# Optimization experiments

Measured on AMD Instinct MI355X. Metric: run time of the kernel, lower is better.

Reference implementation:

```python
import jax, jax.numpy as jnp
import numpy as np

K = 40        # nearest neighbors
BN_EPS = 1e-5  # nn.BatchNorm1d default eps


def _bn(x, g, b):
    # training-mode BatchNorm1d: batch mean, biased variance
    mu = x.mean(0)
    var = x.var(0)
    return g * (x - mu) / jnp.sqrt(var + BN_EPS) + b


def setup_inputs() -> dict:
    key = jax.random.key(0)
    ks = jax.random.split(key, 16)
    N, Cin, D, S, P = 8192, 16, 32, 3, 32

    def w(k, i, o):
        return jax.random.normal(k, (i, o), jnp.float32) * (1.0 / np.sqrt(i))

    return {
        "x": jax.random.normal(ks[0], (N, Cin), jnp.float32),
        "original_coords": jax.random.normal(ks[1], (N, 3), jnp.float32),
        "batch": jnp.zeros((N,), jnp.int32),
        "step_count": 0,
        "num_layer": 1,
        # pre_gravnet MLP
        "pre_w1": w(ks[2], Cin, D), "pre_b1": jnp.zeros((D,), jnp.float32),
        "pre_w2": w(ks[3], D, D), "pre_b2": jnp.zeros((D,), jnp.float32),
        "bn1_g": jnp.ones((D,), jnp.float32), "bn1_b": jnp.zeros((D,), jnp.float32),
        # GravNetConv projections
        "lin_s_w": w(ks[4], D, S),
        "lin_h_w": w(ks[5], D, P), "lin_h_b": jnp.zeros((P,), jnp.float32),
        "lin_w": w(ks[6], D + 2 * P, D), "lin_b": jnp.zeros((D,), jnp.float32),
        # post_gravnet MLP (in = out_channels + space_dims + d_shape = 32+3+32)
        "post_w1": w(ks[7], D + S + D, D), "post_b1": jnp.zeros((D,), jnp.float32),
        "post_w2": w(ks[8], D, D), "post_b2": jnp.zeros((D,), jnp.float32),
        "bn2_g": jnp.ones((D,), jnp.float32), "bn2_b": jnp.zeros((D,), jnp.float32),
    }


def reference(x, original_coords, batch, step_count, num_layer,
              pre_w1, pre_b1, pre_w2, pre_b2, bn1_g, bn1_b,
              lin_s_w, lin_h_w, lin_h_b, lin_w, lin_b,
              post_w1, post_b1, post_w2, post_b2, bn2_g, bn2_b):
    N = x.shape[0]

    # pre_gravnet MLP + batchnorm
    h = jax.nn.elu(x @ pre_w1 + pre_b1)
    h = jax.nn.elu(h @ pre_w2 + pre_b2)
    x_in = _bn(h, bn1_g, bn1_b)

    # GravNetConv projections
    h_l = x_in @ lin_h_w + lin_h_b          # [N, P] propagated features
    s_l = x_in @ lin_s_w                    # [N, S] learned coordinate space

    # kNN graph in s-space (self loops excluded)
    sq = jnp.sum(s_l * s_l, axis=1)
    d2 = sq[:, None] + sq[None, :] - 2.0 * (s_l @ s_l.T)   # [N, N]
    d2 = jnp.maximum(d2, 0.0)
    d2 = jnp.where(jnp.eye(N, dtype=bool), jnp.inf, d2)
    _, idx = jax.lax.top_k(-d2, K)           # [N, K] neighbor indices

    # per-edge squared distance (NOTE: propagate uses the SQUARED distance,
    # faithful to the source where edge_weight is never re-bound to sqrt)
    edge_sq = jnp.take_along_axis(d2, idx, axis=1)    # [N, K]
    dist = jnp.sqrt(edge_sq + 1e-6)                   # [N, K]

    # DGL-side reductions at dst = edge_index[1] = neighbor index
    dst = idx.reshape(-1)
    distf = dist.reshape(-1)
    indeg = jax.ops.segment_sum(jnp.ones_like(distf), dst, num_segments=N)
    sum_d = jax.ops.segment_sum(distf, dst, num_segments=N)
    avdist = jnp.where(indeg > 0, sum_d / jnp.maximum(indeg, 1.0), 0.0)
    loss_regularizing_neig = 0.01 * jnp.mean(jnp.square(avdist - 0.5))

    norm_d = distf / (sum_d + 1e-4)[dst]              # EdgeWeightNorm('right')
    # faithful to source bug: '_edge_w_gndist' is set to the NORMALIZED dist,
    # and apply_edges multiplies by the RAW '_edge_w'
    degs2 = jax.ops.segment_sum(norm_d, dst, num_segments=N) + 1e-4
    gn_final = distf / degs2[dst]
    loss_llregulariser = 0.1 * jnp.mean(jnp.square(norm_d - gn_final))

    # message passing: msg = h_l[neighbor] * squared_dist, mean+max over the
    # K neighbors of each source node (regular fan-in -> dense reduce)
    msgs = h_l[idx] * edge_sq[..., None]              # [N, K, P]
    agg = jnp.concatenate([msgs.mean(1), msgs.max(1)], axis=-1)  # [N, 2P]
    xgn = jnp.concatenate([agg, x_in], axis=-1) @ lin_w + lin_b   # [N, 32]

    # post_gravnet MLP + batchnorm
    cat = jnp.concatenate([xgn, s_l, x_in], axis=1)   # [N, 67]
    o = jax.nn.elu(cat @ post_w1 + post_b1)
    o = jax.nn.elu(o @ post_w2 + post_b2)
    out = _bn(o, bn2_g, bn2_b)
    return (out, loss_regularizing_neig, loss_llregulariser)
```

## Files before the change

### kernel.cpp

```cpp
#include <hip/hip_runtime.h>
#include <math.h>

#define NPTS 8192
#define KNN 40
#define DD 32
#define CIN 16
#define RPB 8
#define CAP 96

#define OFF_H      0u
#define OFF_XIN    262144u
#define OFF_HL     524288u
#define OFF_SL     786432u
#define OFF_ESQ    819200u
#define OFF_O      1146880u
#define OFF_IDX    1409024u
#define OFF_SUMD   1736704u
#define OFF_INDEG  1744896u
#define OFF_STATS  1753088u
#define ZERO_FLOATS (8192u + 8192u + 130u * 32u)

#define ST(i) stats[(i) * 32]

__device__ __forceinline__ float elu_f(float x) { return x > 0.f ? x : (expf(x) - 1.f); }

__device__ __forceinline__ float grp_sum32(float v) {
#pragma unroll
    for (int m = 1; m < 32; m <<= 1) v += __shfl_xor(v, m);
    return v;
}

__device__ __forceinline__ unsigned fkey(float x) {
    unsigned b = __float_as_uint(x);
    return b ^ ((unsigned)((int)b >> 31) | 0x80000000u);
}
__device__ __forceinline__ float kinv(unsigned k) {
    unsigned b = (k & 0x80000000u) ? (k ^ 0x80000000u) : ~k;
    return __uint_as_float(b);
}

__device__ __forceinline__ unsigned bisect_kth(unsigned u0, unsigned u1, int kth) {
    unsigned lo = 0u, hi = 0xFFFFFFFFu;
    while (lo < hi) {
        unsigned mid = lo + ((hi - lo) >> 1);
        int cnt = __popcll(__ballot(u0 <= mid)) + __popcll(__ballot(u1 <= mid));
        if (cnt >= kth) hi = mid; else lo = mid + 1;
    }
    return hi;
}

__global__ __launch_bounds__(256) void k_pre(const float* __restrict__ x,
    const float* __restrict__ w1, const float* __restrict__ b1,
    const float* __restrict__ w2, const float* __restrict__ b2,
    float* __restrict__ h, float* __restrict__ stats)
{
    __shared__ float sw1[CIN * DD], sw2[DD * DD], sb1[DD], sb2[DD];
    __shared__ float bufx[RPB][20], buft[RPB][36];
    __shared__ float sstat[2 * DD];
    int tid = threadIdx.x;
    for (int t = tid; t < CIN * DD; t += 256) sw1[t] = w1[t];
    for (int t = tid; t < DD * DD; t += 256) sw2[t] = w2[t];
    if (tid < DD) { sb1[tid] = b1[tid]; sb2[tid] = b2[tid]; }
    if (tid < 2 * DD) sstat[tid] = 0.f;

    int r = tid >> 5, ch = tid & 31;
    int g = blockIdx.x * RPB + r;
    if (ch < CIN) bufx[r][ch] = x[(size_t)g * CIN + ch];
    __syncthreads();

    float acc = sb1[ch];
#pragma unroll
    for (int k4 = 0; k4 < CIN; k4 += 4) {
        float4 v = *(const float4*)&bufx[r][k4];
        acc = fmaf(v.x, sw1[(k4 + 0) * DD + ch], acc);
        acc = fmaf(v.y, sw1[(k4 + 1) * DD + ch], acc);
        acc = fmaf(v.z, sw1[(k4 + 2) * DD + ch], acc);
        acc = fmaf(v.w, sw1[(k4 + 3) * DD + ch], acc);
    }
    acc = elu_f(acc);
    buft[r][ch] = acc;
    __syncthreads();

    float o = sb2[ch];
#pragma unroll
    for (int k4 = 0; k4 < DD; k4 += 4) {
        float4 v = *(const float4*)&buft[r][k4];
        o = fmaf(v.x, sw2[(k4 + 0) * DD + ch], o);
        o = fmaf(v.y, sw2[(k4 + 1) * DD + ch], o);
        o = fmaf(v.z, sw2[(k4 + 2) * DD + ch], o);
        o = fmaf(v.w, sw2[(k4 + 3) * DD + ch], o);
    }
    o = elu_f(o);
    h[(size_t)g * DD + ch] = o;

    float s = o + __shfl_xor(o, 32);
    float q = o * o;
    q += __shfl_xor(q, 32);
    if ((tid & 32) == 0) { atomicAdd(&sstat[ch], s); atomicAdd(&sstat[DD + ch], q); }
    __syncthreads();
    if (tid < 2 * DD) atomicAdd(&ST(tid), sstat[tid]);
}

__global__ __launch_bounds__(256) void k_proj(const float* __restrict__ h,
    const float* __restrict__ stats,
    const float* __restrict__ g1, const float* __restrict__ b1g,
    const float* __restrict__ hw, const float* __restrict__ hb,
    const float* __restrict__ sw,
    float* __restrict__ xin, float* __restrict__ hl, float4* __restrict__ sl4)
{
    __shared__ float shw[DD * DD], ssw[DD * 3], sa[DD], sbp[DD], shb[DD];
    __shared__ float rrow[RPB][36];
    int tid = threadIdx.x;
    for (int t = tid; t < DD * DD; t += 256) shw[t] = hw[t];
    if (tid < DD * 3) ssw[tid] = sw[tid];
    if (tid < DD) {
        float mean = ST(tid) * (1.f / NPTS);
        float var = ST(32 + tid) * (1.f / NPTS) - mean * mean;
        float a = g1[tid] * rsqrtf(var + 1e-5f);
        sa[tid] = a;
        sbp[tid] = b1g[tid] - a * mean;
        shb[tid] = hb[tid];
    }
    __syncthreads();

    int r = tid >> 5, ch = tid & 31;
    int g = blockIdx.x * RPB + r;

    float v = fmaf(sa[ch], h[(size_t)g * DD + ch], sbp[ch]);
    xin[(size_t)g * DD + ch] = v;
    rrow[r][ch] = v;

    float p0 = v * ssw[ch * 3 + 0];
    float p1 = v * ssw[ch * 3 + 1];
    float p2 = v * ssw[ch * 3 + 2];
    p0 = grp_sum32(p0); p1 = grp_sum32(p1); p2 = grp_sum32(p2);
    if (ch == 0) sl4[g] = make_float4(p0, p1, p2, 0.5f * (p0 * p0 + p1 * p1 + p2 * p2));
    __syncthreads();

    float o = shb[ch];
#pragma unroll
    for (int k4 = 0; k4 < DD; k4 += 4) {
        float4 vv = *(const float4*)&rrow[r][k4];
        o = fmaf(vv.x, shw[(k4 + 0) * DD + ch], o);
        o = fmaf(vv.y, shw[(k4 + 1) * DD + ch], o);
        o = fmaf(vv.z, shw[(k4 + 2) * DD + ch], o);
        o = fmaf(vv.w, shw[(k4 + 3) * DD + ch], o);
    }
    hl[(size_t)g * DD + ch] = o;
}

__device__ __forceinline__ void select_emit(const float2* bufq, int C, int qidx,
    float qw, int lane, int* __restrict__ idxo, float* __restrict__ esq,
    float* __restrict__ sumd, float* __restrict__ indeg)
{
    float e0 = INFINITY, e1 = INFINITY;
    int j0 = -1, j1 = -1;
    if (lane < C) { float2 t = bufq[lane]; e0 = t.x; j0 = __float_as_int(t.y); }
    if (lane + 64 < C) { float2 t = bufq[lane + 64]; e1 = t.x; j1 = __float_as_int(t.y); }
    if (j0 == qidx) e0 = INFINITY;
    if (j1 == qidx) e1 = INFINITY;
    unsigned u0 = fkey(e0), u1 = fkey(e1);
    unsigned thr = bisect_kth(u0, u1, KNN);
    unsigned long long ltm = (1ull << lane) - 1;
    unsigned long long mlt0 = __ballot(u0 < thr), mlt1 = __ballot(u1 < thr);
    unsigned long long meq0 = __ballot(u0 == thr), meq1 = __ballot(u1 == thr);
    int nlt = __popcll(mlt0) + __popcll(mlt1);
    int need = KNN - nlt;
    int rb = qidx * KNN;

    int pos = -1;
    if (u0 < thr) pos = __popcll(mlt0 & ltm);
    else if (u0 == thr) { int rk = __popcll(meq0 & ltm); if (rk < need) pos = nlt + rk; }
    if (pos >= 0) {
        float d2 = fmaxf(2.f * (e0 + qw), 0.f);
        idxo[rb + pos] = j0; esq[rb + pos] = d2;
        float dist = sqrtf(d2 + 1e-6f);
        atomicAdd(&sumd[j0], dist); atomicAdd(&indeg[j0], 1.f);
    }
    pos = -1;
    if (u1 < thr) pos = __popcll(mlt0) + __popcll(mlt1 & ltm);
    else if (u1 == thr) {
        int rk = __popcll(meq0) + __popcll(meq1 & ltm);
        if (rk < need) pos = nlt + rk;
    }
    if (pos >= 0) {
        float d2 = fmaxf(2.f * (e1 + qw), 0.f);
        idxo[rb + pos] = j1; esq[rb + pos] = d2;
        float dist = sqrtf(d2 + 1e-6f);
        atomicAdd(&sumd[j1], dist); atomicAdd(&indeg[j1], 1.f);
    }
}

__global__ __launch_bounds__(256) void k_knn(const float4* __restrict__ sl4,
    int* __restrict__ idxo, float* __restrict__ esq,
    float* __restrict__ sumd, float* __restrict__ indeg)
{
    __shared__ float2 buf[8][CAP];
    int tid = threadIdx.x, lane = tid & 63, wid = tid >> 6;
    int qai = blockIdx.x * 8 + wid * 2;
    int qbi = qai + 1;
    float4 qa = sl4[qai], qb = sl4[qbi];

    float m0a = INFINITY, m1a = INFINITY, m0b = INFINITY, m1b = INFINITY;
    for (int base = 0; base < NPTS; base += 64) {
        float4 p = sl4[base + lane];
        float ea = fmaf(-qa.x, p.x, fmaf(-qa.y, p.y, fmaf(-qa.z, p.z, p.w)));
        float eb = fmaf(-qb.x, p.x, fmaf(-qb.y, p.y, fmaf(-qb.z, p.z, p.w)));
        float lo = fminf(ea, m0a), hi = fmaxf(ea, m0a);
        m0a = lo; m1a = fminf(m1a, hi);
        lo = fminf(eb, m0b); hi = fmaxf(eb, m0b);
        m0b = lo; m1b = fminf(m1b, hi);
    }
    float thrfa = kinv(bisect_kth(fkey(m0a), fkey(m1a), KNN + 1));
    float thrfb = kinv(bisect_kth(fkey(m0b), fkey(m1b), KNN + 1));

    unsigned long long ltm = (1ull << lane) - 1;
    int ca = 0, cbn = 0;
    float2* bufa = buf[wid * 2];
    float2* bufb = buf[wid * 2 + 1];
    for (int base = 0; base < NPTS; base += 64) {
        float4 p = sl4[base + lane];
        int jj = base + lane;
        float ea = fmaf(-qa.x, p.x, fmaf(-qa.y, p.y, fmaf(-qa.z, p.z, p.w)));
        float eb = fmaf(-qb.x, p.x, fmaf(-qb.y, p.y, fmaf(-qb.z, p.z, p.w)));
        unsigned long long ma = __ballot(ea <= thrfa);
        unsigned long long mb = __ballot(eb <= thrfb);
        if (ma) {
            if (ea <= thrfa) {
                int pos = ca + __popcll(ma & ltm);
                if (pos < CAP) bufa[pos] = make_float2(ea, __int_as_float(jj));
            }
            ca += __popcll(ma);
        }
        if (mb) {
            if (eb <= thrfb) {
                int pos = cbn + __popcll(mb & ltm);
                if (pos < CAP) bufb[pos] = make_float2(eb, __int_as_float(jj));
            }
            cbn += __popcll(mb);
        }
    }
    __syncthreads();

    select_emit(bufa, ca < CAP ? ca : CAP, qai, qa.w, lane, idxo, esq, sumd, indeg);
    select_emit(bufb, cbn < CAP ? cbn : CAP, qbi, qb.w, lane, idxo, esq, sumd, indeg);
}

__global__ __launch_bounds__(256) void k_agg(
    const int* __restrict__ idx, const float* __restrict__ esq,
    const float* __restrict__ hl, const float* __restrict__ xin,
    const float4* __restrict__ sl4,
    const float* __restrict__ sumd, const float* __restrict__ indeg,
    const float* __restrict__ lw, const float* __restrict__ lb,
    const float* __restrict__ pw1, const float* __restrict__ pb1,
    const float* __restrict__ pw2, const float* __restrict__ pb2,
    float* __restrict__ o, float* __restrict__ stats)
{
    __shared__ float slw[96 * DD], spw1[67 * DD], spw2[DD * DD];
    __shared__ float slb[DD], spb1[DD], spb2[DD];
    __shared__ float rbuf[RPB][100];
    __shared__ float rb2[RPB][68];
    __shared__ float sstat[2 * DD];
    __shared__ float sl1, sl2;
    int tid = threadIdx.x;
    for (int t = tid; t < 96 * DD; t += 256) slw[t] = lw[t];
    for (int t = tid; t < 67 * DD; t += 256) spw1[t] = pw1[t];
    for (int t = tid; t < DD * DD; t += 256) spw2[t] = pw2[t];
    if (tid < DD) { slb[tid] = lb[tid]; spb1[tid] = pb1[tid]; spb2[tid] = pb2[tid]; }
    if (tid < 2 * DD) sstat[tid] = 0.f;
    if (tid == 254) sl1 = 0.f;
    if (tid == 255) sl2 = 0.f;

    int r = tid >> 5, ch = tid & 31;
    int g = blockIdx.x * RPB + r;
    int rb = g * KNN;

    float sv = 0.f, mv = -INFINITY;
#pragma unroll 8
    for (int k = 0; k < KNN; ++k) {
        int j = idx[rb + k];
        float w = esq[rb + k];
        float m = hl[(size_t)j * DD + ch] * w;
        sv += m;
        mv = fmaxf(mv, m);
    }
    rbuf[r][ch] = sv * (1.f / KNN);
    rbuf[r][32 + ch] = mv;
    rbuf[r][64 + ch] = xin[(size_t)g * DD + ch];
    if (ch == 0) { float4 s = sl4[g]; rbuf[r][96] = s.x; rbuf[r][97] = s.y; rbuf[r][98] = s.z; }
    __syncthreads();

    float l2 = 0.f;
    {
        int j = idx[rb + ch];
        float w = esq[rb + ch];
        float dist = sqrtf(w + 1e-6f);
        float sd = sumd[j];
        float r1 = 1.f / (sd + 1e-4f);
        float dg = sd * r1 + 1e-4f;
        float df = dist * r1 - dist / dg;
        l2 = df * df;
        if (ch < KNN - 32) {
            j = idx[rb + 32 + ch];
            w = esq[rb + 32 + ch];
            dist = sqrtf(w + 1e-6f);
            sd = sumd[j];
            r1 = 1.f / (sd + 1e-4f);
            dg = sd * r1 + 1e-4f;
            df = dist * r1 - dist / dg;
            l2 += df * df;
        }
    }
    l2 = grp_sum32(l2);
    if (ch == 0) {
        float id = indeg[g], sdg = sumd[g];
        float av = id > 0.f ? sdg / fmaxf(id, 1.f) : 0.f;
        float dd = av - 0.5f;
        atomicAdd(&sl2, l2);
        atomicAdd(&sl1, dd * dd);
    }

    float acc = slb[ch];
#pragma unroll
    for (int k4 = 0; k4 < 96; k4 += 4) {
        float4 v = *(const float4*)&rbuf[r][k4];
        acc = fmaf(v.x, slw[(k4 + 0) * DD + ch], acc);
        acc = fmaf(v.y, slw[(k4 + 1) * DD + ch], acc);
        acc = fmaf(v.z, slw[(k4 + 2) * DD + ch], acc);
        acc = fmaf(v.w, slw[(k4 + 3) * DD + ch], acc);
    }
    rb2[r][ch] = acc;
    __syncthreads();

    acc = spb1[ch];
#pragma unroll
    for (int k4 = 0; k4 < DD; k4 += 4) {
        float4 v = *(const float4*)&rb2[r][k4];
        acc = fmaf(v.x, spw1[(k4 + 0) * DD + ch], acc);
        acc = fmaf(v.y, spw1[(k4 + 1) * DD + ch], acc);
        acc = fmaf(v.z, spw1[(k4 + 2) * DD + ch], acc);
        acc = fmaf(v.w, spw1[(k4 + 3) * DD + ch], acc);
    }
#pragma unroll
    for (int s2 = 0; s2 < 3; ++s2)
        acc = fmaf(rbuf[r][96 + s2], spw1[(32 + s2) * DD + ch], acc);
#pragma unroll
    for (int k4 = 0; k4 < DD; k4 += 4) {
        float4 v = *(const float4*)&rbuf[r][64 + k4];
        acc = fmaf(v.x, spw1[(35 + k4 + 0) * DD + ch], acc);
        acc = fmaf(v.y, spw1[(35 + k4 + 1) * DD + ch], acc);
        acc = fmaf(v.z, spw1[(35 + k4 + 2) * DD + ch], acc);
        acc = fmaf(v.w, spw1[(35 + k4 + 3) * DD + ch], acc);
    }
    acc = elu_f(acc);
    rb2[r][32 + ch] = acc;
    __syncthreads();

    acc = spb2[ch];
#pragma unroll
    for (int k4 = 0; k4 < DD; k4 += 4) {
        float4 v = *(const float4*)&rb2[r][32 + k4];
        acc = fmaf(v.x, spw2[(k4 + 0) * DD + ch], acc);
        acc = fmaf(v.y, spw2[(k4 + 1) * DD + ch], acc);
        acc = fmaf(v.z, spw2[(k4 + 2) * DD + ch], acc);
        acc = fmaf(v.w, spw2[(k4 + 3) * DD + ch], acc);
    }
    acc = elu_f(acc);
    o[(size_t)g * DD + ch] = acc;

    float s = acc + __shfl_xor(acc, 32);
    float q = acc * acc;
    q += __shfl_xor(q, 32);
    if ((tid & 32) == 0) { atomicAdd(&sstat[ch], s); atomicAdd(&sstat[DD + ch], q); }
    __syncthreads();
    if (tid < 2 * DD) atomicAdd(&ST(64 + tid), sstat[tid]);
    if (tid == 0) { atomicAdd(&ST(128), sl1); atomicAdd(&ST(129), sl2); }
}

__global__ __launch_bounds__(256) void k_out(const float* __restrict__ o,
    const float* __restrict__ stats, const float* __restrict__ g,
    const float* __restrict__ b, float* __restrict__ dout)
{
    __shared__ float sa[DD], sb[DD];
    int tid = threadIdx.x;
    if (tid < DD) {
        float mean = ST(64 + tid) * (1.f / NPTS);
        float var = ST(96 + tid) * (1.f / NPTS) - mean * mean;
        float a = g[tid] * rsqrtf(var + 1e-5f);
        sa[tid] = a;
        sb[tid] = b[tid] - a * mean;
    }
    __syncthreads();

    int t = blockIdx.x * 256 + tid;
    float4 v = ((const float4*)o)[t];
    int cbase = (t * 4) & (DD - 1);
    float4 rr;
    rr.x = fmaf(sa[cbase + 0], v.x, sb[cbase + 0]);
    rr.y = fmaf(sa[cbase + 1], v.y, sb[cbase + 1]);
    rr.z = fmaf(sa[cbase + 2], v.z, sb[cbase + 2]);
    rr.w = fmaf(sa[cbase + 3], v.w, sb[cbase + 3]);
    ((float4*)dout)[t] = rr;

    if (blockIdx.x == 0) {
        if (tid == DD)     dout[NPTS * DD]     = 0.01f * ST(128) * (1.f / NPTS);
        if (tid == DD + 1) dout[NPTS * DD + 1] = 0.1f  * ST(129) * (1.f / ((float)NPTS * KNN));
    }
}

extern "C" void kernel_launch(void* const* d_in, const int* in_sizes, int n_in,
                              void* d_out, int out_size, void* d_ws, size_t ws_size,
                              hipStream_t stream)
{
    (void)in_sizes; (void)n_in; (void)out_size; (void)ws_size;
    const float* x      = (const float*)d_in[0];
    const float* pre_w1 = (const float*)d_in[5];
    const float* pre_b1 = (const float*)d_in[6];
    const float* pre_w2 = (const float*)d_in[7];
    const float* pre_b2 = (const float*)d_in[8];
    const float* bn1_g  = (const float*)d_in[9];
    const float* bn1_b  = (const float*)d_in[10];
    const float* lin_s_w = (const float*)d_in[11];
    const float* lin_h_w = (const float*)d_in[12];
    const float* lin_h_b = (const float*)d_in[13];
    const float* lin_w   = (const float*)d_in[14];
    const float* lin_b   = (const float*)d_in[15];
    const float* post_w1 = (const float*)d_in[16];
    const float* post_b1 = (const float*)d_in[17];
    const float* post_w2 = (const float*)d_in[18];
    const float* post_b2 = (const float*)d_in[19];
    const float* bn2_g   = (const float*)d_in[20];
    const float* bn2_b   = (const float*)d_in[21];

    float* W = (float*)d_ws;
    float* h     = W + OFF_H;
    float* xin   = W + OFF_XIN;
    float* hl    = W + OFF_HL;
    float4* sl4  = (float4*)(W + OFF_SL);
    float* esq   = W + OFF_ESQ;
    float* o     = W + OFF_O;
    int*   idx   = (int*)(W + OFF_IDX);
    float* sumd  = W + OFF_SUMD;
    float* indeg = W + OFF_INDEG;
    float* stats = W + OFF_STATS;
    float* dout  = (float*)d_out;

    hipMemsetAsync(W + OFF_SUMD, 0, ZERO_FLOATS * sizeof(float), stream);

    k_pre<<<NPTS / RPB, 256, 0, stream>>>(x, pre_w1, pre_b1, pre_w2, pre_b2, h, stats);
    k_proj<<<NPTS / RPB, 256, 0, stream>>>(h, stats, bn1_g, bn1_b,
                                           lin_h_w, lin_h_b, lin_s_w, xin, hl, sl4);
    k_knn<<<NPTS / 8, 256, 0, stream>>>(sl4, idx, esq, sumd, indeg);
    k_agg<<<NPTS / RPB, 256, 0, stream>>>(idx, esq, hl, xin, sl4, sumd, indeg,
                                          lin_w, lin_b, post_w1, post_b1, post_w2, post_b2,
                                          o, stats);
    k_out<<<NPTS * DD / 1024, 256, 0, stream>>>(o, stats, bn2_g, bn2_b, dout);
}
```

Baseline: 131.9 us.

## Stage kNN candidate points in double-buffered LDS tiles, four queries per wave

The kNN kernel now loads the point coordinates into a double-buffered shared-memory tile, with register prefetch of the next tile. Each wave processes four queries instead of two, and the block count is halved. The goal is to cut repeated global/L1 loads of the point array and share each load across more queries. In exchange it uses about 76KB of LDS per block and adds block-wide barriers per tile, which may limit occupancy.

```diff
diff --git a/kernel.cpp b/kernel.cpp
--- a/kernel.cpp
+++ b/kernel.cpp
@@ -7,6 +7,7 @@
 #define CIN 16
 #define RPB 8
 #define CAP 96
+#define TILE 2048
 
 #define OFF_H      0u
 #define OFF_XIN    262144u
@@ -191,59 +192,112 @@
     }
 }
 
+#define EDIST(p, qq) fmaf(-(qq).x, (p).x, fmaf(-(qq).y, (p).y, fmaf(-(qq).z, (p).z, (p).w)))
+
 __global__ __launch_bounds__(256) void k_knn(const float4* __restrict__ sl4,
     int* __restrict__ idxo, float* __restrict__ esq,
     float* __restrict__ sumd, float* __restrict__ indeg)
 {
-    __shared__ float2 buf[8][CAP];
+    __shared__ float4 tile[2][TILE];
+    __shared__ float2 buf[16][CAP];
     int tid = threadIdx.x, lane = tid & 63, wid = tid >> 6;
-    int qai = blockIdx.x * 8 + wid * 2;
-    int qbi = qai + 1;
-    float4 qa = sl4[qai], qb = sl4[qbi];
+    int q0 = blockIdx.x * 16 + wid * 4;
+    float4 qa = sl4[q0], qb = sl4[q0 + 1], qc = sl4[q0 + 2], qd = sl4[q0 + 3];
+
+    float4 st[8];
+#pragma unroll
+    for (int k = 0; k < 8; ++k) st[k] = sl4[k * 256 + tid];
+#pragma unroll
+    for (int k = 0; k < 8; ++k) tile[0][k * 256 + tid] = st[k];
+    __syncthreads();
 
     float m0a = INFINITY, m1a = INFINITY, m0b = INFINITY, m1b = INFINITY;
-    for (int base = 0; base < NPTS; base += 64) {
-        float4 p = sl4[base + lane];
-        float ea = fmaf(-qa.x, p.x, fmaf(-qa.y, p.y, fmaf(-qa.z, p.z, p.w)));
-        float eb = fmaf(-qb.x, p.x, fmaf(-qb.y, p.y, fmaf(-qb.z, p.z, p.w)));
-        float lo = fminf(ea, m0a), hi = fmaxf(ea, m0a);
-        m0a = lo; m1a = fminf(m1a, hi);
-        lo = fminf(eb, m0b); hi = fmaxf(eb, m0b);
-        m0b = lo; m1b = fminf(m1b, hi);
+    float m0c = INFINITY, m1c = INFINITY, m0d = INFINITY, m1d = INFINITY;
+
+#define TOP2Q(p, qq, m0, m1) { \
+        float e = EDIST(p, qq); \
+        float lo = fminf(e, m0), hi = fmaxf(e, m0); \
+        m0 = lo; m1 = fminf(m1, hi); }
+
+    for (int t = 0; t < NPTS / TILE; ++t) {
+        if (t + 1 < NPTS / TILE) {
+#pragma unroll
+            for (int k = 0; k < 8; ++k) st[k] = sl4[(t + 1) * TILE + k * 256 + tid];
+        }
+        const float4* tp = tile[t & 1];
+#pragma unroll 4
+        for (int g = 0; g < TILE / 64; ++g) {
+            float4 p = tp[g * 64 + lane];
+            TOP2Q(p, qa, m0a, m1a)
+            TOP2Q(p, qb, m0b, m1b)
+            TOP2Q(p, qc, m0c, m1c)
+            TOP2Q(p, qd, m0d, m1d)
+        }
+        __syncthreads();
+        if (t + 1 < NPTS / TILE) {
+#pragma unroll
+            for (int k = 0; k < 8; ++k) tile[(t + 1) & 1][k * 256 + tid] = st[k];
+        }
+        __syncthreads();
     }
     float thrfa = kinv(bisect_kth(fkey(m0a), fkey(m1a), KNN + 1));
     float thrfb = kinv(bisect_kth(fkey(m0b), fkey(m1b), KNN + 1));
+    float thrfc = kinv(bisect_kth(fkey(m0c), fkey(m1c), KNN + 1));
+    float thrfd = kinv(bisect_kth(fkey(m0d), fkey(m1d), KNN + 1));
 
     unsigned long long ltm = (1ull << lane) - 1;
-    int ca = 0, cbn = 0;
-    float2* bufa = buf[wid * 2];
-    float2* bufb = buf[wid * 2 + 1];
-    for (int base = 0; base < NPTS; base += 64) {
-        float4 p = sl4[base + lane];
-        int jj = base + lane;
-        float ea = fmaf(-qa.x, p.x, fmaf(-qa.y, p.y, fmaf(-qa.z, p.z, p.w)));
-        float eb = fmaf(-qb.x, p.x, fmaf(-qb.y, p.y, fmaf(-qb.z, p.z, p.w)));
-        unsigned long long ma = __ballot(ea <= thrfa);
-        unsigned long long mb = __ballot(eb <= thrfb);
-        if (ma) {
-            if (ea <= thrfa) {
-                int pos = ca + __popcll(ma & ltm);
-                if (pos < CAP) bufa[pos] = make_float2(ea, __int_as_float(jj));
-            }
-            ca += __popcll(ma);
-        }
-        if (mb) {
-            if (eb <= thrfb) {
-                int pos = cbn + __popcll(mb & ltm);
-                if (pos < CAP) bufb[pos] = make_float2(eb, __int_as_float(jj));
-            }
-            cbn += __popcll(mb);
-        }
-    }
-    __syncthreads();
-
-    select_emit(bufa, ca < CAP ? ca : CAP, qai, qa.w, lane, idxo, esq, sumd, indeg);
-    select_emit(bufb, cbn < CAP ? cbn : CAP, qbi, qb.w, lane, idxo, esq, sumd, indeg);
+    int ca = 0, cb = 0, cc = 0, cd = 0;
+    float2* bufa = buf[wid * 4 + 0];
+    float2* bufb = buf[wid * 4 + 1];
+    float2* bufc = buf[wid * 4 + 2];
+    float2* bufd = buf[wid * 4 + 3];
+
+#define COLL(e, thrv, cnt, brow, jj) { \
+        unsigned long long mm = __ballot((e) <= (thrv)); \
+        if (mm) { \
+            if ((e) <= (thrv)) { \
+                int pos = cnt + __popcll(mm & ltm); \
+                if (pos < CAP) brow[pos] = make_float2((e), __int_as_float(jj)); \
+            } \
+            cnt += __popcll(mm); \
+        } }
+
+#pragma unroll
+    for (int k = 0; k < 8; ++k) st[k] = sl4[k * 256 + tid];
+#pragma unroll
+    for (int k = 0; k < 8; ++k) tile[0][k * 256 + tid] = st[k];
+    __syncthreads();
+
+    for (int t = 0; t < NPTS / TILE; ++t) {
+        if (t + 1 < NPTS / TILE) {
+#pragma unroll
+            for (int k = 0; k < 8; ++k) st[k] = sl4[(t + 1) * TILE + k * 256 + tid];
+        }
+        const float4* tp = tile[t & 1];
+        int tbase = t * TILE;
+#pragma unroll 4
+        for (int g = 0; g < TILE / 64; ++g) {
+            float4 p = tp[g * 64 + lane];
+            int jj = tbase + g * 64 + lane;
+            float ea = EDIST(p, qa), eb = EDIST(p, qb);
+            float ec = EDIST(p, qc), ed = EDIST(p, qd);
+            COLL(ea, thrfa, ca, bufa, jj)
+            COLL(eb, thrfb, cb, bufb, jj)
+            COLL(ec, thrfc, cc, bufc, jj)
+            COLL(ed, thrfd, cd, bufd, jj)
+        }
+        __syncthreads();
+        if (t + 1 < NPTS / TILE) {
+#pragma unroll
+            for (int k = 0; k < 8; ++k) tile[(t + 1) & 1][k * 256 + tid] = st[k];
+        }
+        __syncthreads();
+    }
+
+    select_emit(bufa, ca < CAP ? ca : CAP, q0 + 0, qa.w, lane, idxo, esq, sumd, indeg);
+    select_emit(bufb, cb < CAP ? cb : CAP, q0 + 1, qb.w, lane, idxo, esq, sumd, indeg);
+    select_emit(bufc, cc < CAP ? cc : CAP, q0 + 2, qc.w, lane, idxo, esq, sumd, indeg);
+    select_emit(bufd, cd < CAP ? cd : CAP, q0 + 3, qd.w, lane, idxo, esq, sumd, indeg);
 }
 
 __global__ __launch_bounds__(256) void k_agg(
@@ -450,7 +504,7 @@
     k_pre<<<NPTS / RPB, 256, 0, stream>>>(x, pre_w1, pre_b1, pre_w2, pre_b2, h, stats);
     k_proj<<<NPTS / RPB, 256, 0, stream>>>(h, stats, bn1_g, bn1_b,
                                            lin_h_w, lin_h_b, lin_s_w, xin, hl, sl4);
-    k_knn<<<NPTS / 8, 256, 0, stream>>>(sl4, idx, esq, sumd, indeg);
+    k_knn<<<NPTS / 16, 256, 0, stream>>>(sl4, idx, esq, sumd, indeg);
     k_agg<<<NPTS / RPB, 256, 0, stream>>>(idx, esq, hl, xin, sl4, sumd, indeg,
                                           lin_w, lin_b, post_w1, post_b1, post_w2, post_b2,
                                           o, stats);
```

Measured after the change: 147.4 us. +11.7%, slower.

## Split kNN candidate scan across two waves per query pair

Applied to the files above, without the earlier changes.

The kNN kernel now assigns each pair of queries to two wavefronts, each scanning half the points, and merges per-lane top-2 minima through shared memory to compute a joint threshold. Each half then collects candidates into a 64-entry buffer, and one wave per query runs the final selection over both halves. This halves the serial scan length per wave and doubles the grid size to expose more parallelism. The cost is an extra block barrier and a per-half candidate cap of 64, which could drop true neighbours if one half holds many ties near the threshold.

```diff
diff --git a/kernel.cpp b/kernel.cpp
--- a/kernel.cpp
+++ b/kernel.cpp
@@ -6,7 +6,8 @@
 #define DD 32
 #define CIN 16
 #define RPB 8
-#define CAP 96
+#define HALF 4096
+#define CAP2 64
 
 #define OFF_H      0u
 #define OFF_XIN    262144u
@@ -44,6 +45,18 @@
     while (lo < hi) {
         unsigned mid = lo + ((hi - lo) >> 1);
         int cnt = __popcll(__ballot(u0 <= mid)) + __popcll(__ballot(u1 <= mid));
+        if (cnt >= kth) hi = mid; else lo = mid + 1;
+    }
+    return hi;
+}
+
+__device__ __forceinline__ unsigned bisect_kth4(unsigned u0, unsigned u1,
+    unsigned u2, unsigned u3, int kth) {
+    unsigned lo = 0u, hi = 0xFFFFFFFFu;
+    while (lo < hi) {
+        unsigned mid = lo + ((hi - lo) >> 1);
+        int cnt = __popcll(__ballot(u0 <= mid)) + __popcll(__ballot(u1 <= mid))
+                + __popcll(__ballot(u2 <= mid)) + __popcll(__ballot(u3 <= mid));
         if (cnt >= kth) hi = mid; else lo = mid + 1;
     }
     return hi;
@@ -149,14 +162,15 @@
     hl[(size_t)g * DD + ch] = o;
 }
 
-__device__ __forceinline__ void select_emit(const float2* bufq, int C, int qidx,
-    float qw, int lane, int* __restrict__ idxo, float* __restrict__ esq,
+__device__ __forceinline__ void select_emit2(const float2* buf0, int c0,
+    const float2* buf1, int c1, int qidx, float qw, int lane,
+    int* __restrict__ idxo, float* __restrict__ esq,
     float* __restrict__ sumd, float* __restrict__ indeg)
 {
     float e0 = INFINITY, e1 = INFINITY;
     int j0 = -1, j1 = -1;
-    if (lane < C) { float2 t = bufq[lane]; e0 = t.x; j0 = __float_as_int(t.y); }
-    if (lane + 64 < C) { float2 t = bufq[lane + 64]; e1 = t.x; j1 = __float_as_int(t.y); }
+    if (lane < c0) { float2 t = buf0[lane]; e0 = t.x; j0 = __float_as_int(t.y); }
+    if (lane < c1) { float2 t = buf1[lane]; e1 = t.x; j1 = __float_as_int(t.y); }
     if (j0 == qidx) e0 = INFINITY;
     if (j1 == qidx) e1 = INFINITY;
     unsigned u0 = fkey(e0), u1 = fkey(e1);
@@ -191,59 +205,75 @@
     }
 }
 
+#define EDIST(p, qq) fmaf(-(qq).x, (p).x, fmaf(-(qq).y, (p).y, fmaf(-(qq).z, (p).z, (p).w)))
+
 __global__ __launch_bounds__(256) void k_knn(const float4* __restrict__ sl4,
     int* __restrict__ idxo, float* __restrict__ esq,
     float* __restrict__ sumd, float* __restrict__ indeg)
 {
-    __shared__ float2 buf[8][CAP];
+    __shared__ float2 pool[4][2][64];
+    __shared__ float2 cand[4][2][CAP2];
+    __shared__ int cnts[4][2];
     int tid = threadIdx.x, lane = tid & 63, wid = tid >> 6;
-    int qai = blockIdx.x * 8 + wid * 2;
-    int qbi = qai + 1;
+    int p = wid >> 1, h = wid & 1;
+    int qbase = blockIdx.x * 4;
+    int qai = qbase + 2 * p, qbi = qai + 1;
     float4 qa = sl4[qai], qb = sl4[qbi];
+    int pbase = h * HALF;
 
     float m0a = INFINITY, m1a = INFINITY, m0b = INFINITY, m1b = INFINITY;
-    for (int base = 0; base < NPTS; base += 64) {
-        float4 p = sl4[base + lane];
-        float ea = fmaf(-qa.x, p.x, fmaf(-qa.y, p.y, fmaf(-qa.z, p.z, p.w)));
-        float eb = fmaf(-qb.x, p.x, fmaf(-qb.y, p.y, fmaf(-qb.z, p.z, p.w)));
-        float lo = fminf(ea, m0a), hi = fmaxf(ea, m0a);
-        m0a = lo; m1a = fminf(m1a, hi);
-        lo = fminf(eb, m0b); hi = fmaxf(eb, m0b);
-        m0b = lo; m1b = fminf(m1b, hi);
-    }
-    float thrfa = kinv(bisect_kth(fkey(m0a), fkey(m1a), KNN + 1));
-    float thrfb = kinv(bisect_kth(fkey(m0b), fkey(m1b), KNN + 1));
+
+#define TOP2Q(pt, qq, m0, m1) { \
+        float e = EDIST(pt, qq); \
+        float lo = fminf(e, m0), hi = fmaxf(e, m0); \
+        m0 = lo; m1 = fminf(m1, hi); }
+
+    for (int i = 0; i < HALF; i += 64) {
+        float4 pt = sl4[pbase + i + lane];
+        TOP2Q(pt, qa, m0a, m1a)
+        TOP2Q(pt, qb, m0b, m1b)
+    }
+    pool[2 * p][h][lane] = make_float2(m0a, m1a);
+    pool[2 * p + 1][h][lane] = make_float2(m0b, m1b);
+    __syncthreads();
+
+    float2 a0 = pool[2 * p][0][lane], a1 = pool[2 * p][1][lane];
+    float2 b0 = pool[2 * p + 1][0][lane], b1 = pool[2 * p + 1][1][lane];
+    float thra = kinv(bisect_kth4(fkey(a0.x), fkey(a0.y), fkey(a1.x), fkey(a1.y), KNN + 1));
+    float thrb = kinv(bisect_kth4(fkey(b0.x), fkey(b0.y), fkey(b1.x), fkey(b1.y), KNN + 1));
 
     unsigned long long ltm = (1ull << lane) - 1;
-    int ca = 0, cbn = 0;
-    float2* bufa = buf[wid * 2];
-    float2* bufb = buf[wid * 2 + 1];
-    for (int base = 0; base < NPTS; base += 64) {
-        float4 p = sl4[base + lane];
-        int jj = base + lane;
-        float ea = fmaf(-qa.x, p.x, fmaf(-qa.y, p.y, fmaf(-qa.z, p.z, p.w)));
-        float eb = fmaf(-qb.x, p.x, fmaf(-qb.y, p.y, fmaf(-qb.z, p.z, p.w)));
-        unsigned long long ma = __ballot(ea <= thrfa);
-        unsigned long long mb = __ballot(eb <= thrfb);
-        if (ma) {
-            if (ea <= thrfa) {
-                int pos = ca + __popcll(ma & ltm);
-                if (pos < CAP) bufa[pos] = make_float2(ea, __int_as_float(jj));
-            }
-            ca += __popcll(ma);
-        }
-        if (mb) {
-            if (eb <= thrfb) {
-                int pos = cbn + __popcll(mb & ltm);
-                if (pos < CAP) bufb[pos] = make_float2(eb, __int_as_float(jj));
-            }
-            cbn += __popcll(mb);
-        }
-    }
-    __syncthreads();
-
-    select_emit(bufa, ca < CAP ? ca : CAP, qai, qa.w, lane, idxo, esq, sumd, indeg);
-    select_emit(bufb, cbn < CAP ? cbn : CAP, qbi, qb.w, lane, idxo, esq, sumd, indeg);
+    int ca = 0, cb = 0;
+    float2* bufa = cand[2 * p][h];
+    float2* bufb = cand[2 * p + 1][h];
+
+#define COLL(e, thrv, cnt, brow, jj) { \
+        unsigned long long mm = __ballot((e) <= (thrv)); \
+        if (mm) { \
+            if ((e) <= (thrv)) { \
+                int pos = cnt + __popcll(mm & ltm); \
+                if (pos < CAP2) brow[pos] = make_float2((e), __int_as_float(jj)); \
+            } \
+            cnt += __popcll(mm); \
+        } }
+
+    for (int i = 0; i < HALF; i += 64) {
+        float4 pt = sl4[pbase + i + lane];
+        int jj = pbase + i + lane;
+        float ea = EDIST(pt, qa), eb = EDIST(pt, qb);
+        COLL(ea, thra, ca, bufa, jj)
+        COLL(eb, thrb, cb, bufb, jj)
+    }
+    if (lane == 0) {
+        cnts[2 * p][h] = ca < CAP2 ? ca : CAP2;
+        cnts[2 * p + 1][h] = cb < CAP2 ? cb : CAP2;
+    }
+    __syncthreads();
+
+    int qi = qbase + wid;
+    float qw = sl4[qi].w;
+    select_emit2(cand[wid][0], cnts[wid][0], cand[wid][1], cnts[wid][1],
+                 qi, qw, lane, idxo, esq, sumd, indeg);
 }
 
 __global__ __launch_bounds__(256) void k_agg(
@@ -450,7 +480,7 @@
     k_pre<<<NPTS / RPB, 256, 0, stream>>>(x, pre_w1, pre_b1, pre_w2, pre_b2, h, stats);
     k_proj<<<NPTS / RPB, 256, 0, stream>>>(h, stats, bn1_g, bn1_b,
                                            lin_h_w, lin_h_b, lin_s_w, xin, hl, sl4);
-    k_knn<<<NPTS / 8, 256, 0, stream>>>(sl4, idx, esq, sumd, indeg);
+    k_knn<<<NPTS / 4, 256, 0, stream>>>(sl4, idx, esq, sumd, indeg);
     k_agg<<<NPTS / RPB, 256, 0, stream>>>(idx, esq, hl, xin, sl4, sumd, indeg,
                                           lin_w, lin_b, post_w1, post_b1, post_w2, post_b2,
                                           o, stats);
```

Result: faster. 122.6 us (-7.1%).

## Split kNN point scan across waves with 8 queries per wave register tile

Applied to the files above, without the earlier changes.

Reorganises the kNN kernel so each wave scans a quarter of the points for all 8 block queries, instead of all points for 2 queries. Per-lane minima from the four waves are pooled in shared memory to compute each query's candidate threshold, and per-quarter candidate lists are merged in a 4-way selection. This amortises point loads over more queries and shortens each wave's serial loop. In exchange it raises register pressure and lowers per-quarter candidate capacity to 64, which could drop neighbours on skewed distributions.

```diff
diff --git a/kernel.cpp b/kernel.cpp
--- a/kernel.cpp
+++ b/kernel.cpp
@@ -6,7 +6,9 @@
 #define DD 32
 #define CIN 16
 #define RPB 8
-#define CAP 96
+#define QPB 8
+#define QTR 2048
+#define CAP3 64
 
 #define OFF_H      0u
 #define OFF_XIN    262144u
@@ -39,11 +41,13 @@
     return __uint_as_float(b);
 }
 
-__device__ __forceinline__ unsigned bisect_kth(unsigned u0, unsigned u1, int kth) {
+__device__ __forceinline__ unsigned bisect_kth4(unsigned u0, unsigned u1,
+    unsigned u2, unsigned u3, int kth) {
     unsigned lo = 0u, hi = 0xFFFFFFFFu;
     while (lo < hi) {
         unsigned mid = lo + ((hi - lo) >> 1);
-        int cnt = __popcll(__ballot(u0 <= mid)) + __popcll(__ballot(u1 <= mid));
+        int cnt = __popcll(__ballot(u0 <= mid)) + __popcll(__ballot(u1 <= mid))
+                + __popcll(__ballot(u2 <= mid)) + __popcll(__ballot(u3 <= mid));
         if (cnt >= kth) hi = mid; else lo = mid + 1;
     }
     return hi;
@@ -149,101 +153,149 @@
     hl[(size_t)g * DD + ch] = o;
 }
 
-__device__ __forceinline__ void select_emit(const float2* bufq, int C, int qidx,
-    float qw, int lane, int* __restrict__ idxo, float* __restrict__ esq,
+__device__ __forceinline__ void emit_one(unsigned u, int j, float qw,
+    unsigned thr, int nlt, int need, int prelt, int preeq,
+    unsigned long long mlt, unsigned long long meq, unsigned long long ltm,
+    int rb, int* __restrict__ idxo, float* __restrict__ esq,
     float* __restrict__ sumd, float* __restrict__ indeg)
 {
-    float e0 = INFINITY, e1 = INFINITY;
-    int j0 = -1, j1 = -1;
-    if (lane < C) { float2 t = bufq[lane]; e0 = t.x; j0 = __float_as_int(t.y); }
-    if (lane + 64 < C) { float2 t = bufq[lane + 64]; e1 = t.x; j1 = __float_as_int(t.y); }
+    int pos = -1;
+    if (u < thr) pos = prelt + __popcll(mlt & ltm);
+    else if (u == thr) {
+        int rk = preeq + __popcll(meq & ltm);
+        if (rk < need) pos = nlt + rk;
+    }
+    if (pos >= 0) {
+        float e = kinv(u);
+        float d2 = fmaxf(2.f * (e + qw), 0.f);
+        idxo[rb + pos] = j; esq[rb + pos] = d2;
+        float dist = sqrtf(d2 + 1e-6f);
+        atomicAdd(&sumd[j], dist); atomicAdd(&indeg[j], 1.f);
+    }
+}
+
+__device__ __forceinline__ void select_emit4(
+    const float2* b0, int c0, const float2* b1, int c1,
+    const float2* b2, int c2, const float2* b3, int c3,
+    int qidx, float qw, int lane,
+    int* __restrict__ idxo, float* __restrict__ esq,
+    float* __restrict__ sumd, float* __restrict__ indeg)
+{
+    float e0 = INFINITY, e1 = INFINITY, e2 = INFINITY, e3 = INFINITY;
+    int j0 = -1, j1 = -1, j2 = -1, j3 = -1;
+    if (lane < c0) { float2 t = b0[lane]; e0 = t.x; j0 = __float_as_int(t.y); }
+    if (lane < c1) { float2 t = b1[lane]; e1 = t.x; j1 = __float_as_int(t.y); }
+    if (lane < c2) { float2 t = b2[lane]; e2 = t.x; j2 = __float_as_int(t.y); }
+    if (lane < c3) { float2 t = b3[lane]; e3 = t.x; j3 = __float_as_int(t.y); }
     if (j0 == qidx) e0 = INFINITY;
     if (j1 == qidx) e1 = INFINITY;
-    unsigned u0 = fkey(e0), u1 = fkey(e1);
-    unsigned thr = bisect_kth(u0, u1, KNN);
+    if (j2 == qidx) e2 = INFINITY;
+    if (j3 == qidx) e3 = INFINITY;
+    unsigned u0 = fkey(e0), u1 = fkey(e1), u2 = fkey(e2), u3 = fkey(e3);
+    unsigned thr = bisect_kth4(u0, u1, u2, u3, KNN);
     unsigned long long ltm = (1ull << lane) - 1;
     unsigned long long mlt0 = __ballot(u0 < thr), mlt1 = __ballot(u1 < thr);
+    unsigned long long mlt2 = __ballot(u2 < thr), mlt3 = __ballot(u3 < thr);
     unsigned long long meq0 = __ballot(u0 == thr), meq1 = __ballot(u1 == thr);
-    int nlt = __popcll(mlt0) + __popcll(mlt1);
+    unsigned long long meq2 = __ballot(u2 == thr), meq3 = __ballot(u3 == thr);
+    int n0 = __popcll(mlt0), n1 = __popcll(mlt1), n2 = __popcll(mlt2), n3 = __popcll(mlt3);
+    int q0 = __popcll(meq0), q1 = __popcll(meq1), q2 = __popcll(meq2);
+    int nlt = n0 + n1 + n2 + n3;
     int need = KNN - nlt;
     int rb = qidx * KNN;
 
-    int pos = -1;
-    if (u0 < thr) pos = __popcll(mlt0 & ltm);
-    else if (u0 == thr) { int rk = __popcll(meq0 & ltm); if (rk < need) pos = nlt + rk; }
-    if (pos >= 0) {
-        float d2 = fmaxf(2.f * (e0 + qw), 0.f);
-        idxo[rb + pos] = j0; esq[rb + pos] = d2;
-        float dist = sqrtf(d2 + 1e-6f);
-        atomicAdd(&sumd[j0], dist); atomicAdd(&indeg[j0], 1.f);
-    }
-    pos = -1;
-    if (u1 < thr) pos = __popcll(mlt0) + __popcll(mlt1 & ltm);
-    else if (u1 == thr) {
-        int rk = __popcll(meq0) + __popcll(meq1 & ltm);
-        if (rk < need) pos = nlt + rk;
-    }
-    if (pos >= 0) {
-        float d2 = fmaxf(2.f * (e1 + qw), 0.f);
-        idxo[rb + pos] = j1; esq[rb + pos] = d2;
-        float dist = sqrtf(d2 + 1e-6f);
-        atomicAdd(&sumd[j1], dist); atomicAdd(&indeg[j1], 1.f);
-    }
-}
+    emit_one(u0, j0, qw, thr, nlt, need, 0, 0, mlt0, meq0, ltm, rb, idxo, esq, sumd, indeg);
+    emit_one(u1, j1, qw, thr, nlt, need, n0, q0, mlt1, meq1, ltm, rb, idxo, esq, sumd, indeg);
+    emit_one(u2, j2, qw, thr, nlt, need, n0 + n1, q0 + q1, mlt2, meq2, ltm, rb, idxo, esq, sumd, indeg);
+    emit_one(u3, j3, qw, thr, nlt, need, n0 + n1 + n2, q0 + q1 + q2, mlt3, meq3, ltm, rb, idxo, esq, sumd, indeg);
+}
+
+#define EDIST8(pt, q) fmaf(-qx[q], (pt).x, fmaf(-qy[q], (pt).y, fmaf(-qz[q], (pt).z, (pt).w)))
 
 __global__ __launch_bounds__(256) void k_knn(const float4* __restrict__ sl4,
     int* __restrict__ idxo, float* __restrict__ esq,
     float* __restrict__ sumd, float* __restrict__ indeg)
 {
-    __shared__ float2 buf[8][CAP];
-    int tid = threadIdx.x, lane = tid & 63, wid = tid >> 6;
-    int qai = blockIdx.x * 8 + wid * 2;
-    int qbi = qai + 1;
-    float4 qa = sl4[qai], qb = sl4[qbi];
-
-    float m0a = INFINITY, m1a = INFINITY, m0b = INFINITY, m1b = INFINITY;
-    for (int base = 0; base < NPTS; base += 64) {
-        float4 p = sl4[base + lane];
-        float ea = fmaf(-qa.x, p.x, fmaf(-qa.y, p.y, fmaf(-qa.z, p.z, p.w)));
-        float eb = fmaf(-qb.x, p.x, fmaf(-qb.y, p.y, fmaf(-qb.z, p.z, p.w)));
-        float lo = fminf(ea, m0a), hi = fmaxf(ea, m0a);
-        m0a = lo; m1a = fminf(m1a, hi);
-        lo = fminf(eb, m0b); hi = fmaxf(eb, m0b);
-        m0b = lo; m1b = fminf(m1b, hi);
-    }
-    float thrfa = kinv(bisect_kth(fkey(m0a), fkey(m1a), KNN + 1));
-    float thrfb = kinv(bisect_kth(fkey(m0b), fkey(m1b), KNN + 1));
+    __shared__ float pool[QPB][4][64];
+    __shared__ float2 cand[QPB][4][CAP3];
+    __shared__ int cnts[QPB][4];
+    __shared__ float sthr[QPB];
+    int tid = threadIdx.x, lane = tid & 63, w = tid >> 6;
+    int qbase = blockIdx.x * QPB;
+
+    float qx[QPB], qy[QPB], qz[QPB];
+#pragma unroll
+    for (int q = 0; q < QPB; ++q) {
+        float4 t = sl4[qbase + q];
+        qx[q] = t.x; qy[q] = t.y; qz[q] = t.z;
+    }
+    int pbase = w * QTR;
+    int rot = blockIdx.x & (QTR / 64 - 1);
+
+    float m0[QPB];
+#pragma unroll
+    for (int q = 0; q < QPB; ++q) m0[q] = INFINITY;
+
+    for (int i = 0; i < QTR / 64; ++i) {
+        int chunk = (i + rot) & (QTR / 64 - 1);
+        float4 pt = sl4[pbase + chunk * 64 + lane];
+#pragma unroll
+        for (int q = 0; q < QPB; ++q) m0[q] = fminf(m0[q], EDIST8(pt, q));
+    }
+#pragma unroll
+    for (int q = 0; q < QPB; ++q) pool[q][w][lane] = m0[q];
+    __syncthreads();
+
+#pragma unroll
+    for (int k = 0; k < 2; ++k) {
+        int q = 2 * w + k;
+        unsigned t = bisect_kth4(fkey(pool[q][0][lane]), fkey(pool[q][1][lane]),
+                                 fkey(pool[q][2][lane]), fkey(pool[q][3][lane]), KNN + 1);
+        if (lane == 0) sthr[q] = kinv(t);
+    }
+    __syncthreads();
+
+    float thr[QPB];
+#pragma unroll
+    for (int q = 0; q < QPB; ++q) thr[q] = sthr[q];
 
     unsigned long long ltm = (1ull << lane) - 1;
-    int ca = 0, cbn = 0;
-    float2* bufa = buf[wid * 2];
-    float2* bufb = buf[wid * 2 + 1];
-    for (int base = 0; base < NPTS; base += 64) {
-        float4 p = sl4[base + lane];
-        int jj = base + lane;
-        float ea = fmaf(-qa.x, p.x, fmaf(-qa.y, p.y, fmaf(-qa.z, p.z, p.w)));
-        float eb = fmaf(-qb.x, p.x, fmaf(-qb.y, p.y, fmaf(-qb.z, p.z, p.w)));
-        unsigned long long ma = __ballot(ea <= thrfa);
-        unsigned long long mb = __ballot(eb <= thrfb);
-        if (ma) {
-            if (ea <= thrfa) {
-                int pos = ca + __popcll(ma & ltm);
-                if (pos < CAP) bufa[pos] = make_float2(ea, __int_as_float(jj));
+    int cnt[QPB];
+#pragma unroll
+    for (int q = 0; q < QPB; ++q) cnt[q] = 0;
+
+    for (int i = 0; i < QTR / 64; ++i) {
+        int chunk = (i + rot) & (QTR / 64 - 1);
+        int jj = pbase + chunk * 64 + lane;
+        float4 pt = sl4[jj];
+#pragma unroll
+        for (int q = 0; q < QPB; ++q) {
+            float e = EDIST8(pt, q);
+            unsigned long long mm = __ballot(e <= thr[q]);
+            if (mm) {
+                if (e <= thr[q]) {
+                    int pos = cnt[q] + __popcll(mm & ltm);
+                    if (pos < CAP3) cand[q][w][pos] = make_float2(e, __int_as_float(jj));
+                }
+                cnt[q] += __popcll(mm);
             }
-            ca += __popcll(ma);
         }
-        if (mb) {
-            if (eb <= thrfb) {
-                int pos = cbn + __popcll(mb & ltm);
-                if (pos < CAP) bufb[pos] = make_float2(eb, __int_as_float(jj));
-            }
-            cbn += __popcll(mb);
-        }
-    }
-    __syncthreads();
-
-    select_emit(bufa, ca < CAP ? ca : CAP, qai, qa.w, lane, idxo, esq, sumd, indeg);
-    select_emit(bufb, cbn < CAP ? cbn : CAP, qbi, qb.w, lane, idxo, esq, sumd, indeg);
+    }
+    if (lane == 0) {
+#pragma unroll
+        for (int q = 0; q < QPB; ++q) cnts[q][w] = cnt[q] < CAP3 ? cnt[q] : CAP3;
+    }
+    __syncthreads();
+
+#pragma unroll
+    for (int k = 0; k < 2; ++k) {
+        int q = 2 * w + k;
+        int qi = qbase + q;
+        float qw_ = sl4[qi].w;
+        select_emit4(cand[q][0], cnts[q][0], cand[q][1], cnts[q][1],
+                     cand[q][2], cnts[q][2], cand[q][3], cnts[q][3],
+                     qi, qw_, lane, idxo, esq, sumd, indeg);
+    }
 }
 
 __global__ __launch_bounds__(256) void k_agg(
@@ -450,7 +502,7 @@
     k_pre<<<NPTS / RPB, 256, 0, stream>>>(x, pre_w1, pre_b1, pre_w2, pre_b2, h, stats);
     k_proj<<<NPTS / RPB, 256, 0, stream>>>(h, stats, bn1_g, bn1_b,
                                            lin_h_w, lin_h_b, lin_s_w, xin, hl, sl4);
-    k_knn<<<NPTS / 8, 256, 0, stream>>>(sl4, idx, esq, sumd, indeg);
+    k_knn<<<NPTS / QPB, 256, 0, stream>>>(sl4, idx, esq, sumd, indeg);
     k_agg<<<NPTS / RPB, 256, 0, stream>>>(idx, esq, hl, xin, sl4, sumd, indeg,
                                           lin_w, lin_b, post_w1, post_b1, post_w2, post_b2,
                                           o, stats);
```

Result: faster. 122.9 us (-6.8%).
